# Kernel optimization log

Hardware: AMD Instinct MI355X
Metric: run time of the kernel (lower is better)

The kernel has to match this reference:

```python
import jax, jax.numpy as jnp
import numpy as np

N_NODES = 100000
N_EDGES = 1600000
N_CLASS = 45


def gcn_conv(x, W, b, src, dst, ew, n):
    # PyG GCNConv: add self-loops (weight 1), symmetric deg^-1/2 normalization,
    # linear transform, scatter-add aggregation into targets, then bias.
    loops = jnp.arange(n, dtype=src.dtype)
    s = jnp.concatenate([src, loops])
    d = jnp.concatenate([dst, loops])
    w = jnp.concatenate([ew, jnp.ones((n,), ew.dtype)])
    deg = jax.ops.segment_sum(w, d, num_segments=n)          # in-degree (weighted)
    dis = jnp.where(deg > 0, 1.0 / jnp.sqrt(deg), 0.0)      # deg^-1/2, 0 where deg==0
    norm = dis[s] * w * dis[d]                               # [E+n]
    h = x @ W                                                # [n, out]
    out = jax.ops.segment_sum(h[s] * norm[:, None], d, num_segments=n)
    return out + b


def setup_inputs() -> dict:
    key = jax.random.key(0)
    ks = jax.random.split(key, 6)
    x = jax.random.normal(ks[0], (N_NODES, N_CLASS), dtype=jnp.float32)
    edge_src = jax.random.randint(ks[1], (N_EDGES,), 0, N_NODES, dtype=jnp.int64 if jax.config.jax_enable_x64 else jnp.int32).astype(jnp.int32)
    edge_dst = jax.random.randint(ks[2], (N_EDGES,), 0, N_NODES, dtype=jnp.int64 if jax.config.jax_enable_x64 else jnp.int32).astype(jnp.int32)
    edge_w = jax.random.uniform(ks[3], (N_EDGES,), dtype=jnp.float32)
    W1 = jax.random.normal(ks[4], (N_CLASS, 32), dtype=jnp.float32) / np.sqrt(N_CLASS)
    b1 = jnp.zeros((32,), dtype=jnp.float32)
    W2 = jax.random.normal(ks[5], (32, 128), dtype=jnp.float32) / np.sqrt(32.0)
    b2 = jnp.zeros((128,), dtype=jnp.float32)
    return {"x": x, "edge_src": edge_src, "edge_dst": edge_dst, "edge_w": edge_w,
            "W1": W1, "b1": b1, "W2": W2, "b2": b2}


def reference(x, edge_src, edge_dst, edge_w, W1, b1, W2, b2):
    n = x.shape[0]
    h = jnp.tanh(gcn_conv(x, W1, b1, edge_src, edge_dst, edge_w, n))
    return gcn_conv(h, W2, b2, edge_src, edge_dst, edge_w, n)
```

## Files before the change

kernel.cpp:

```cpp
#include <hip/hip_runtime.h>
#include <hip/hip_fp16.h>
#include <math.h>

static constexpr int TPB = 256;
static constexpr int NPB_SHIFT = 8;
static constexpr int BCAP = 5120;
static constexpr int PCHUNK = 4096;

__device__ __forceinline__ int p_src(unsigned p) { return (int)(p >> 15); }
__device__ __forceinline__ float p_w(unsigned p) {
  return __half2float(__ushort_as_half((unsigned short)(p & 0x7FFFu)));
}

struct h2x4 { __half2 a, b, c, d; };

__device__ __forceinline__ __half2 shfl_h2(__half2 v, int mask) {
  int b = *reinterpret_cast<int*>(&v);
  int r = __shfl_xor(b, mask, 64);
  return *reinterpret_cast<__half2*>(&r);
}

__global__ void k_partition(const int* __restrict__ src, const int* __restrict__ dst,
                            const float* __restrict__ ew, int* __restrict__ bkcnt,
                            unsigned* __restrict__ ppk, unsigned char* __restrict__ pld,
                            int E, int NB) {
  __shared__ int lh[512];
  __shared__ int lbase[512];
  __shared__ int lcur[512];
  int tid = threadIdx.x;
  long long e0 = (long long)blockIdx.x * PCHUNK;
  int d[PCHUNK / TPB];
  unsigned pk[PCHUNK / TPB];
  for (int t = tid; t < NB; t += TPB) { lh[t] = 0; lcur[t] = 0; }
  __syncthreads();
#pragma unroll
  for (int r = 0; r < PCHUNK / TPB; ++r) {
    long long e = e0 + (long long)r * TPB + tid;
    if (e < E) {
      d[r] = dst[e];
      pk[r] = ((unsigned)src[e] << 15) |
              ((unsigned)__half_as_ushort(__float2half(ew[e])) & 0x7FFFu);
      atomicAdd(&lh[d[r] >> NPB_SHIFT], 1);
    } else {
      d[r] = -1;
    }
  }
  __syncthreads();
  for (int t = tid; t < NB; t += TPB)
    lbase[t] = lh[t] ? (t * BCAP + atomicAdd(&bkcnt[t], lh[t])) : 0;
  __syncthreads();
#pragma unroll
  for (int r = 0; r < PCHUNK / TPB; ++r) {
    if (d[r] >= 0) {
      int b = d[r] >> NPB_SHIFT;
      int pos = atomicAdd(&lcur[b], 1);
      size_t gp = (size_t)lbase[b] + pos;
      ppk[gp] = pk[r];
      pld[gp] = (unsigned char)(d[r] & 255);
    }
  }
}

__global__ void __launch_bounds__(TPB) k_bucket(const unsigned* __restrict__ ppk,
                                                const unsigned char* __restrict__ pld,
                                                const int* __restrict__ bkcnt,
                                                unsigned* __restrict__ csr,
                                                int2* __restrict__ rc,
                                                float* __restrict__ dis,
                                                const float* __restrict__ x,
                                                const float* __restrict__ W1,
                                                __half2* __restrict__ hh, int n) {
  __shared__ unsigned lpk[BCAP];
  __shared__ unsigned char lld[BCAP];
  __shared__ float sW[45 * 32];
  __shared__ int lcnt[256];
  __shared__ int lofs[256];
  __shared__ float lsum[256];
  int b = blockIdx.x;
  int t = threadIdx.x;
  int beg = b * BCAP;
  int m = bkcnt[b];
  if (m > BCAP) m = BCAP;
  lcnt[t] = 0;
  lsum[t] = 0.f;
  for (int i = t; i < 45 * 32; i += TPB) sW[i] = W1[i];
  __syncthreads();
  for (int i = t; i < m; i += TPB) {
    unsigned pk = ppk[(size_t)beg + i];
    unsigned char ld = pld[(size_t)beg + i];
    lpk[i] = pk;
    lld[i] = ld;
    atomicAdd(&lcnt[ld], 1);
  }
  __syncthreads();
  int v = lcnt[t];
  lofs[t] = v;
  __syncthreads();
  for (int off = 1; off < 256; off <<= 1) {
    int tv = (t >= off) ? lofs[t - off] : 0;
    __syncthreads();
    lofs[t] += tv;
    __syncthreads();
  }
  int ex = lofs[t] - v;
  int gnode = (b << NPB_SHIFT) + t;
  if (gnode < n) rc[gnode] = make_int2(beg + ex, v);
  lcnt[t] = ex;
  __syncthreads();
  for (int i = t; i < m; i += TPB) {
    unsigned pk = lpk[i];
    int ld = lld[i];
    int pos = atomicAdd(&lcnt[ld], 1);
    csr[(size_t)beg + pos] = pk;
    atomicAdd(&lsum[ld], p_w(pk));
  }
  __syncthreads();
  if (gnode < n) {
    float dsc = rsqrtf(1.0f + lsum[t]);
    dis[gnode] = dsc;
    float xr[45];
#pragma unroll
    for (int k = 0; k < 45; ++k) xr[k] = x[(size_t)gnode * 45 + k];
    __half2* hw = hh + (size_t)gnode * 16;
#pragma unroll 2
    for (int j2 = 0; j2 < 16; ++j2) {
      float a0 = 0.f, a1 = 0.f;
#pragma unroll
      for (int k = 0; k < 45; ++k) {
        a0 = fmaf(xr[k], sW[k * 32 + j2 * 2], a0);
        a1 = fmaf(xr[k], sW[k * 32 + j2 * 2 + 1], a1);
      }
      hw[j2] = __floats2half2_rn(a0 * dsc, a1 * dsc);
    }
  }
}

__global__ void k_gather1(const unsigned* __restrict__ csr, const int2* __restrict__ rc,
                          const float* __restrict__ dis, const __half2* __restrict__ hh,
                          const float* __restrict__ b1, __half2* __restrict__ outv, int n) {
  int gid = blockIdx.x * blockDim.x + threadIdx.x;
  int node = gid >> 2;
  if (node >= n) return;
  int q = (threadIdx.x & 3) * 4;
  int2 r = rc[node];
  const unsigned* row = csr + r.x;
  int m = r.y;
  const __half2* tbl = hh + q;
  float2 c0 = {0.f, 0.f}, c1 = {0.f, 0.f}, c2 = {0.f, 0.f}, c3 = {0.f, 0.f};
  float2 d0 = {0.f, 0.f}, d1 = {0.f, 0.f}, d2 = {0.f, 0.f}, d3 = {0.f, 0.f};
  int e = 0;
  for (; e + 3 < m; e += 4) {
    unsigned p0 = row[e], p1 = row[e + 1], p2 = row[e + 2], p3 = row[e + 3];
    h2x4 v0 = *reinterpret_cast<const h2x4*>(tbl + (size_t)p_src(p0) * 16);
    h2x4 v1 = *reinterpret_cast<const h2x4*>(tbl + (size_t)p_src(p1) * 16);
    h2x4 v2 = *reinterpret_cast<const h2x4*>(tbl + (size_t)p_src(p2) * 16);
    h2x4 v3 = *reinterpret_cast<const h2x4*>(tbl + (size_t)p_src(p3) * 16);
    float w0 = p_w(p0), w1 = p_w(p1), w2 = p_w(p2), w3 = p_w(p3);
    float2 f;
    f = __half22float2(v0.a); c0.x = fmaf(w0, f.x, c0.x); c0.y = fmaf(w0, f.y, c0.y);
    f = __half22float2(v0.b); c1.x = fmaf(w0, f.x, c1.x); c1.y = fmaf(w0, f.y, c1.y);
    f = __half22float2(v0.c); c2.x = fmaf(w0, f.x, c2.x); c2.y = fmaf(w0, f.y, c2.y);
    f = __half22float2(v0.d); c3.x = fmaf(w0, f.x, c3.x); c3.y = fmaf(w0, f.y, c3.y);
    f = __half22float2(v1.a); d0.x = fmaf(w1, f.x, d0.x); d0.y = fmaf(w1, f.y, d0.y);
    f = __half22float2(v1.b); d1.x = fmaf(w1, f.x, d1.x); d1.y = fmaf(w1, f.y, d1.y);
    f = __half22float2(v1.c); d2.x = fmaf(w1, f.x, d2.x); d2.y = fmaf(w1, f.y, d2.y);
    f = __half22float2(v1.d); d3.x = fmaf(w1, f.x, d3.x); d3.y = fmaf(w1, f.y, d3.y);
    f = __half22float2(v2.a); c0.x = fmaf(w2, f.x, c0.x); c0.y = fmaf(w2, f.y, c0.y);
    f = __half22float2(v2.b); c1.x = fmaf(w2, f.x, c1.x); c1.y = fmaf(w2, f.y, c1.y);
    f = __half22float2(v2.c); c2.x = fmaf(w2, f.x, c2.x); c2.y = fmaf(w2, f.y, c2.y);
    f = __half22float2(v2.d); c3.x = fmaf(w2, f.x, c3.x); c3.y = fmaf(w2, f.y, c3.y);
    f = __half22float2(v3.a); d0.x = fmaf(w3, f.x, d0.x); d0.y = fmaf(w3, f.y, d0.y);
    f = __half22float2(v3.b); d1.x = fmaf(w3, f.x, d1.x); d1.y = fmaf(w3, f.y, d1.y);
    f = __half22float2(v3.c); d2.x = fmaf(w3, f.x, d2.x); d2.y = fmaf(w3, f.y, d2.y);
    f = __half22float2(v3.d); d3.x = fmaf(w3, f.x, d3.x); d3.y = fmaf(w3, f.y, d3.y);
  }
  for (; e < m; ++e) {
    unsigned p = row[e];
    h2x4 v = *reinterpret_cast<const h2x4*>(tbl + (size_t)p_src(p) * 16);
    float w = p_w(p);
    float2 f;
    f = __half22float2(v.a); c0.x = fmaf(w, f.x, c0.x); c0.y = fmaf(w, f.y, c0.y);
    f = __half22float2(v.b); c1.x = fmaf(w, f.x, c1.x); c1.y = fmaf(w, f.y, c1.y);
    f = __half22float2(v.c); c2.x = fmaf(w, f.x, c2.x); c2.y = fmaf(w, f.y, c2.y);
    f = __half22float2(v.d); c3.x = fmaf(w, f.x, c3.x); c3.y = fmaf(w, f.y, c3.y);
  }
  c0.x += d0.x; c0.y += d0.y; c1.x += d1.x; c1.y += d1.y;
  c2.x += d2.x; c2.y += d2.y; c3.x += d3.x; c3.y += d3.y;
  float dd = dis[node];
  h2x4 own = *reinterpret_cast<const h2x4*>(hh + (size_t)node * 16 + q);
  __half2* op = outv + (size_t)node * 16 + q;
  float2 o0 = __half22float2(own.a), o1 = __half22float2(own.b);
  float2 o2 = __half22float2(own.c), o3 = __half22float2(own.d);
  const float4* bp = reinterpret_cast<const float4*>(b1 + q * 2);
  float4 ba = bp[0], bb = bp[1];
  op[0] = __floats2half2_rn(dd * tanhf(ba.x + dd * (c0.x + o0.x)),
                            dd * tanhf(ba.y + dd * (c0.y + o0.y)));
  op[1] = __floats2half2_rn(dd * tanhf(ba.z + dd * (c1.x + o1.x)),
                            dd * tanhf(ba.w + dd * (c1.y + o1.y)));
  op[2] = __floats2half2_rn(dd * tanhf(bb.x + dd * (c2.x + o2.x)),
                            dd * tanhf(bb.y + dd * (c2.y + o2.y)));
  op[3] = __floats2half2_rn(dd * tanhf(bb.z + dd * (c3.x + o3.x)),
                            dd * tanhf(bb.w + dd * (c3.y + o3.y)));
}

__global__ void k_gather2g(const unsigned* __restrict__ csr, const int2* __restrict__ rc,
                           const float* __restrict__ dis, const __half2* __restrict__ hh,
                           const float* __restrict__ W2, const float* __restrict__ b2,
                           float* __restrict__ out, int n) {
  __shared__ float sW[32 * 128];
  __shared__ float sB[128];
  for (int t = threadIdx.x; t < 32 * 128; t += blockDim.x) sW[t] = W2[t];
  if (threadIdx.x < 128) sB[threadIdx.x] = b2[threadIdx.x];
  __syncthreads();
  int gid = blockIdx.x * blockDim.x + threadIdx.x;
  int node = gid >> 2;
  if (node >= n) return;
  int lq = threadIdx.x & 3;
  int q = lq * 4;
  int2 r = rc[node];
  const unsigned* row = csr + r.x;
  int m = r.y;
  const __half2* tbl = hh + q;
  float2 c0 = {0.f, 0.f}, c1 = {0.f, 0.f}, c2 = {0.f, 0.f}, c3 = {0.f, 0.f};
  float2 d0 = {0.f, 0.f}, d1 = {0.f, 0.f}, d2 = {0.f, 0.f}, d3 = {0.f, 0.f};
  int e = 0;
  for (; e + 3 < m; e += 4) {
    unsigned p0 = row[e], p1 = row[e + 1], p2 = row[e + 2], p3 = row[e + 3];
    h2x4 v0 = *reinterpret_cast<const h2x4*>(tbl + (size_t)p_src(p0) * 16);
    h2x4 v1 = *reinterpret_cast<const h2x4*>(tbl + (size_t)p_src(p1) * 16);
    h2x4 v2 = *reinterpret_cast<const h2x4*>(tbl + (size_t)p_src(p2) * 16);
    h2x4 v3 = *reinterpret_cast<const h2x4*>(tbl + (size_t)p_src(p3) * 16);
    float w0 = p_w(p0), w1 = p_w(p1), w2 = p_w(p2), w3 = p_w(p3);
    float2 f;
    f = __half22float2(v0.a); c0.x = fmaf(w0, f.x, c0.x); c0.y = fmaf(w0, f.y, c0.y);
    f = __half22float2(v0.b); c1.x = fmaf(w0, f.x, c1.x); c1.y = fmaf(w0, f.y, c1.y);
    f = __half22float2(v0.c); c2.x = fmaf(w0, f.x, c2.x); c2.y = fmaf(w0, f.y, c2.y);
    f = __half22float2(v0.d); c3.x = fmaf(w0, f.x, c3.x); c3.y = fmaf(w0, f.y, c3.y);
    f = __half22float2(v1.a); d0.x = fmaf(w1, f.x, d0.x); d0.y = fmaf(w1, f.y, d0.y);
    f = __half22float2(v1.b); d1.x = fmaf(w1, f.x, d1.x); d1.y = fmaf(w1, f.y, d1.y);
    f = __half22float2(v1.c); d2.x = fmaf(w1, f.x, d2.x); d2.y = fmaf(w1, f.y, d2.y);
    f = __half22float2(v1.d); d3.x = fmaf(w1, f.x, d3.x); d3.y = fmaf(w1, f.y, d3.y);
    f = __half22float2(v2.a); c0.x = fmaf(w2, f.x, c0.x); c0.y = fmaf(w2, f.y, c0.y);
    f = __half22float2(v2.b); c1.x = fmaf(w2, f.x, c1.x); c1.y = fmaf(w2, f.y, c1.y);
    f = __half22float2(v2.c); c2.x = fmaf(w2, f.x, c2.x); c2.y = fmaf(w2, f.y, c2.y);
    f = __half22float2(v2.d); c3.x = fmaf(w2, f.x, c3.x); c3.y = fmaf(w2, f.y, c3.y);
    f = __half22float2(v3.a); d0.x = fmaf(w3, f.x, d0.x); d0.y = fmaf(w3, f.y, d0.y);
    f = __half22float2(v3.b); d1.x = fmaf(w3, f.x, d1.x); d1.y = fmaf(w3, f.y, d1.y);
    f = __half22float2(v3.c); d2.x = fmaf(w3, f.x, d2.x); d2.y = fmaf(w3, f.y, d2.y);
    f = __half22float2(v3.d); d3.x = fmaf(w3, f.x, d3.x); d3.y = fmaf(w3, f.y, d3.y);
  }
  for (; e < m; ++e) {
    unsigned p = row[e];
    h2x4 v = *reinterpret_cast<const h2x4*>(tbl + (size_t)p_src(p) * 16);
    float w = p_w(p);
    float2 f;
    f = __half22float2(v.a); c0.x = fmaf(w, f.x, c0.x); c0.y = fmaf(w, f.y, c0.y);
    f = __half22float2(v.b); c1.x = fmaf(w, f.x, c1.x); c1.y = fmaf(w, f.y, c1.y);
    f = __half22float2(v.c); c2.x = fmaf(w, f.x, c2.x); c2.y = fmaf(w, f.y, c2.y);
    f = __half22float2(v.d); c3.x = fmaf(w, f.x, c3.x); c3.y = fmaf(w, f.y, c3.y);
  }
  float dd = dis[node];
  h2x4 own = *reinterpret_cast<const h2x4*>(hh + (size_t)node * 16 + q);
  float2 o0 = __half22float2(own.a), o1 = __half22float2(own.b);
  float2 o2 = __half22float2(own.c), o3 = __half22float2(own.d);
  __half2 y0 = __floats2half2_rn(dd * (c0.x + d0.x + o0.x), dd * (c0.y + d0.y + o0.y));
  __half2 y1 = __floats2half2_rn(dd * (c1.x + d1.x + o1.x), dd * (c1.y + d1.y + o1.y));
  __half2 y2 = __floats2half2_rn(dd * (c2.x + d2.x + o2.x), dd * (c2.y + d2.y + o2.y));
  __half2 y3 = __floats2half2_rn(dd * (c3.x + d3.x + o3.x), dd * (c3.y + d3.y + o3.y));
  __half2 g1_0 = shfl_h2(y0, 1), g1_1 = shfl_h2(y1, 1), g1_2 = shfl_h2(y2, 1), g1_3 = shfl_h2(y3, 1);
  __half2 g2_0 = shfl_h2(y0, 2), g2_1 = shfl_h2(y1, 2), g2_2 = shfl_h2(y2, 2), g2_3 = shfl_h2(y3, 2);
  __half2 g3_0 = shfl_h2(y0, 3), g3_1 = shfl_h2(y1, 3), g3_2 = shfl_h2(y2, 3), g3_3 = shfl_h2(y3, 3);
  int g4 = lq * 4;
  float4 a[8];
#pragma unroll
  for (int qq = 0; qq < 8; ++qq) a[qq] = *reinterpret_cast<const float4*>(&sB[g4 + qq * 16]);
#define GEMM_GRP(kb, h0, h1, h2v, h3v)                                              \
  {                                                                                 \
    __half2 hv[4] = {h0, h1, h2v, h3v};                                             \
    _Pragma("unroll") for (int i = 0; i < 4; ++i) {                                 \
      float2 yv = __half22float2(hv[i]);                                            \
      const float* w0 = &sW[((kb + i) * 2) * 128 + g4];                             \
      const float* w1 = &sW[((kb + i) * 2 + 1) * 128 + g4];                         \
      _Pragma("unroll") for (int qq = 0; qq < 8; ++qq) {                            \
        float4 wa = *reinterpret_cast<const float4*>(w0 + qq * 16);                 \
        float4 wb = *reinterpret_cast<const float4*>(w1 + qq * 16);                 \
        a[qq].x = fmaf(yv.x, wa.x, fmaf(yv.y, wb.x, a[qq].x));                      \
        a[qq].y = fmaf(yv.x, wa.y, fmaf(yv.y, wb.y, a[qq].y));                      \
        a[qq].z = fmaf(yv.x, wa.z, fmaf(yv.y, wb.z, a[qq].z));                      \
        a[qq].w = fmaf(yv.x, wa.w, fmaf(yv.y, wb.w, a[qq].w));                      \
      }                                                                             \
    }                                                                               \
  }
  GEMM_GRP(lq * 4, y0, y1, y2, y3)
  GEMM_GRP((lq ^ 1) * 4, g1_0, g1_1, g1_2, g1_3)
  GEMM_GRP((lq ^ 2) * 4, g2_0, g2_1, g2_2, g2_3)
  GEMM_GRP((lq ^ 3) * 4, g3_0, g3_1, g3_2, g3_3)
#undef GEMM_GRP
  float* op = out + (size_t)node * 128 + g4;
#pragma unroll
  for (int qq = 0; qq < 8; ++qq) *reinterpret_cast<float4*>(op + qq * 16) = a[qq];
}

static inline dim3 gx(long long work) { return dim3((unsigned)((work + TPB - 1) / TPB)); }

extern "C" void kernel_launch(void* const* d_in, const int* in_sizes, int n_in,
                              void* d_out, int out_size, void* d_ws, size_t ws_size,
                              hipStream_t stream) {
  const float* x   = (const float*)d_in[0];
  const int*   src = (const int*)d_in[1];
  const int*   dst = (const int*)d_in[2];
  const float* ew  = (const float*)d_in[3];
  const float* W1  = (const float*)d_in[4];
  const float* b1  = (const float*)d_in[5];
  const float* W2  = (const float*)d_in[6];
  const float* b2  = (const float*)d_in[7];
  float* out = (float*)d_out;

  const int n = in_sizes[0] / 45;
  const int E = in_sizes[1];
  const int NB = (n + 255) >> NPB_SHIFT;

  char* w = (char*)d_ws;
  size_t o = 0;
  auto alloc = [&](size_t bytes) { void* p = w + o; o += ((bytes + 255) & ~(size_t)255); return p; };
  int*           bkcnt = (int*)          alloc((size_t)NB * 4);
  unsigned*      ppk   = (unsigned*)     alloc((size_t)NB * BCAP * 4);
  unsigned char* pld   = (unsigned char*)alloc((size_t)NB * BCAP);
  unsigned*      csr   = (unsigned*)     alloc((size_t)NB * BCAP * 4);
  int2*          rc    = (int2*)         alloc((size_t)n * 8);
  float*         dis   = (float*)        alloc((size_t)n * 4);
  __half2*       hh    = (__half2*)      alloc((size_t)n * 32 * 2);
  __half2*       ag1   = (__half2*)      alloc((size_t)n * 32 * 2);

  const int PB = (E + PCHUNK - 1) / PCHUNK;

  hipMemsetAsync(bkcnt, 0, (size_t)NB * 4, stream);
  k_partition<<<PB, TPB, 0, stream>>>(src, dst, ew, bkcnt, ppk, pld, E, NB);
  k_bucket<<<NB, TPB, 0, stream>>>(ppk, pld, bkcnt, csr, rc, dis, x, W1, hh, n);
  k_gather1<<<gx((long long)n * 4), TPB, 0, stream>>>(csr, rc, dis, hh, b1, ag1, n);
  k_gather2g<<<gx((long long)n * 4), TPB, 0, stream>>>(csr, rc, dis, ag1, W2, b2, out, n);
}
```

Measured before the change: 141.4 us.

## Sort nodes by degree within each bucket to balance gather wavefronts

The bucket kernel now builds a per-block counting sort of nodes by in-degree (descending, capped at 62) and writes a permutation array. Both gather kernels walk nodes in this order, so the lanes of a wavefront handle nodes with similar edge counts and wait less on the longest row. In exchange the gathers pay an extra indirection, and output writes and row reads become less contiguous.

```diff
diff --git a/kernel.cpp b/kernel.cpp
--- a/kernel.cpp
+++ b/kernel.cpp
@@ -69,13 +69,16 @@
                                                 float* __restrict__ dis,
                                                 const float* __restrict__ x,
                                                 const float* __restrict__ W1,
-                                                __half2* __restrict__ hh, int n) {
+                                                __half2* __restrict__ hh,
+                                                int* __restrict__ gord, int n) {
   __shared__ unsigned lpk[BCAP];
   __shared__ unsigned char lld[BCAP];
   __shared__ float sW[45 * 32];
   __shared__ int lcnt[256];
   __shared__ int lofs[256];
   __shared__ float lsum[256];
+  __shared__ int dbin[64];
+  __shared__ int dbase[64];
   int b = blockIdx.x;
   int t = threadIdx.x;
   int beg = b * BCAP;
@@ -83,6 +86,7 @@
   if (m > BCAP) m = BCAP;
   lcnt[t] = 0;
   lsum[t] = 0.f;
+  if (t < 64) dbin[t] = 0;
   for (int i = t; i < 45 * 32; i += TPB) sW[i] = W1[i];
   __syncthreads();
   for (int i = t; i < m; i += TPB) {
@@ -105,8 +109,14 @@
   int ex = lofs[t] - v;
   int gnode = (b << NPB_SHIFT) + t;
   if (gnode < n) rc[gnode] = make_int2(beg + ex, v);
+  int vv = (gnode < n) ? (min(v, 62) + 1) : 0;
+  atomicAdd(&dbin[vv], 1);
   lcnt[t] = ex;
   __syncthreads();
+  if (t == 0) {
+    int run = 0;
+    for (int d2 = 63; d2 >= 0; --d2) { dbase[d2] = run; run += dbin[d2]; }
+  }
   for (int i = t; i < m; i += TPB) {
     unsigned pk = lpk[i];
     int ld = lld[i];
@@ -115,6 +125,8 @@
     atomicAdd(&lsum[ld], p_w(pk));
   }
   __syncthreads();
+  int rnk = atomicAdd(&dbase[vv], 1);
+  gord[(b << NPB_SHIFT) + rnk] = (gnode < n) ? gnode : -1;
   if (gnode < n) {
     float dsc = rsqrtf(1.0f + lsum[t]);
     dis[gnode] = dsc;
@@ -137,10 +149,13 @@
 
 __global__ void k_gather1(const unsigned* __restrict__ csr, const int2* __restrict__ rc,
                           const float* __restrict__ dis, const __half2* __restrict__ hh,
-                          const float* __restrict__ b1, __half2* __restrict__ outv, int n) {
+                          const float* __restrict__ b1, __half2* __restrict__ outv,
+                          const int* __restrict__ gord, int NT) {
   int gid = blockIdx.x * blockDim.x + threadIdx.x;
-  int node = gid >> 2;
-  if (node >= n) return;
+  int i = gid >> 2;
+  if (i >= NT) return;
+  int node = gord[i];
+  if (node < 0) return;
   int q = (threadIdx.x & 3) * 4;
   int2 r = rc[node];
   const unsigned* row = csr + r.x;
@@ -206,15 +221,17 @@
 __global__ void k_gather2g(const unsigned* __restrict__ csr, const int2* __restrict__ rc,
                            const float* __restrict__ dis, const __half2* __restrict__ hh,
                            const float* __restrict__ W2, const float* __restrict__ b2,
-                           float* __restrict__ out, int n) {
+                           float* __restrict__ out, const int* __restrict__ gord, int NT) {
   __shared__ float sW[32 * 128];
   __shared__ float sB[128];
   for (int t = threadIdx.x; t < 32 * 128; t += blockDim.x) sW[t] = W2[t];
   if (threadIdx.x < 128) sB[threadIdx.x] = b2[threadIdx.x];
   __syncthreads();
   int gid = blockIdx.x * blockDim.x + threadIdx.x;
-  int node = gid >> 2;
-  if (node >= n) return;
+  int i = gid >> 2;
+  if (i >= NT) return;
+  int node = gord[i];
+  if (node < 0) return;
   int lq = threadIdx.x & 3;
   int q = lq * 4;
   int2 r = rc[node];
@@ -277,10 +294,10 @@
 #define GEMM_GRP(kb, h0, h1, h2v, h3v)                                              \
   {                                                                                 \
     __half2 hv[4] = {h0, h1, h2v, h3v};                                             \
-    _Pragma("unroll") for (int i = 0; i < 4; ++i) {                                 \
-      float2 yv = __half22float2(hv[i]);                                            \
-      const float* w0 = &sW[((kb + i) * 2) * 128 + g4];                             \
-      const float* w1 = &sW[((kb + i) * 2 + 1) * 128 + g4];                         \
+    _Pragma("unroll") for (int ii = 0; ii < 4; ++ii) {                              \
+      float2 yv = __half22float2(hv[ii]);                                           \
+      const float* w0 = &sW[((kb + ii) * 2) * 128 + g4];                            \
+      const float* w1 = &sW[((kb + ii) * 2 + 1) * 128 + g4];                        \
       _Pragma("unroll") for (int qq = 0; qq < 8; ++qq) {                            \
         float4 wa = *reinterpret_cast<const float4*>(w0 + qq * 16);                 \
         float4 wb = *reinterpret_cast<const float4*>(w1 + qq * 16);                 \
@@ -319,6 +336,7 @@
   const int n = in_sizes[0] / 45;
   const int E = in_sizes[1];
   const int NB = (n + 255) >> NPB_SHIFT;
+  const int NT = NB << NPB_SHIFT;
 
   char* w = (char*)d_ws;
   size_t o = 0;
@@ -329,6 +347,7 @@
   unsigned*      csr   = (unsigned*)     alloc((size_t)NB * BCAP * 4);
   int2*          rc    = (int2*)         alloc((size_t)n * 8);
   float*         dis   = (float*)        alloc((size_t)n * 4);
+  int*           gord  = (int*)          alloc((size_t)NT * 4);
   __half2*       hh    = (__half2*)      alloc((size_t)n * 32 * 2);
   __half2*       ag1   = (__half2*)      alloc((size_t)n * 32 * 2);
 
@@ -336,7 +355,7 @@
 
   hipMemsetAsync(bkcnt, 0, (size_t)NB * 4, stream);
   k_partition<<<PB, TPB, 0, stream>>>(src, dst, ew, bkcnt, ppk, pld, E, NB);
-  k_bucket<<<NB, TPB, 0, stream>>>(ppk, pld, bkcnt, csr, rc, dis, x, W1, hh, n);
-  k_gather1<<<gx((long long)n * 4), TPB, 0, stream>>>(csr, rc, dis, hh, b1, ag1, n);
-  k_gather2g<<<gx((long long)n * 4), TPB, 0, stream>>>(csr, rc, dis, ag1, W2, b2, out, n);
-}
+  k_bucket<<<NB, TPB, 0, stream>>>(ppk, pld, bkcnt, csr, rc, dis, x, W1, hh, gord, n);
+  k_gather1<<<gx((long long)NT * 4), TPB, 0, stream>>>(csr, rc, dis, hh, b1, ag1, gord, NT);
+  k_gather2g<<<gx((long long)NT * 4), TPB, 0, stream>>>(csr, rc, dis, ag1, W2, b2, out, gord, NT);
+}
```

Measured after the change: 154.9 us. 9.6% more time.
